# Kernel optimization log

Hardware: AMD Instinct MI355X
Metric: run time of the kernel (lower is better)

The kernel has to match this reference:

```python
import jax, jax.numpy as jnp
import numpy as np

N, E, G, D, L, T = 50000, 100000, 2000, 300, 5, 10
NUM_ATOM, NUM_CHIR, NUM_BOND, NUM_DIR = 120, 3, 6, 3


def setup_inputs() -> dict:
    key = jax.random.key(0)
    ks = jax.random.split(key, 24)
    s = 1.0 / np.sqrt(D)
    inp = {
        'x': jnp.stack([jax.random.randint(ks[0], (N,), 0, NUM_ATOM),
                        jax.random.randint(ks[1], (N,), 0, NUM_CHIR)], axis=1),
        'edge_index': jax.random.randint(ks[2], (2, E), 0, N),
        'edge_attr': jnp.stack([jax.random.randint(ks[3], (E,), 0, 4),
                                jax.random.randint(ks[4], (E,), 0, NUM_DIR)], axis=1),
        'batch': jnp.sort(jax.random.randint(ks[5], (N,), 0, G)),
        'x1': jnp.stack([jax.random.randint(ks[6], (N,), 0, NUM_ATOM),
                         jax.random.randint(ks[7], (N,), 0, NUM_CHIR)], axis=1),
        'edge_index1': jax.random.randint(ks[8], (2, E), 0, N),
        'edge_attr1': jnp.stack([jax.random.randint(ks[9], (E,), 0, 4),
                                 jax.random.randint(ks[10], (E,), 0, NUM_DIR)], axis=1),
        'batch1': jnp.sort(jax.random.randint(ks[11], (N,), 0, G)),
        'xemb1': jax.random.normal(ks[12], (NUM_ATOM, D)) * s,
        'xemb2': jax.random.normal(ks[13], (NUM_CHIR, D)) * s,
        'eemb1': jax.random.normal(ks[14], (L, NUM_BOND, D)) * s,
        'eemb2': jax.random.normal(ks[15], (L, NUM_DIR, D)) * s,
        'W1': jax.random.normal(ks[16], (L, D, 2 * D)) * s,
        'b1': jnp.zeros((L, 2 * D)),
        'W2': jax.random.normal(ks[17], (L, 2 * D, D)) * (1.0 / np.sqrt(2 * D)),
        'b2': jnp.zeros((L, D)),
        'gamma': jnp.ones((L, D)),
        'beta': jnp.zeros((L, D)),
        'predW': jax.random.normal(ks[18], (D, T)) * s,
        'predb': jnp.zeros((T,)),
    }
    return inp


def _gnn(xi, ei, ea, xemb1, xemb2, eemb1, eemb2, W1, b1, W2, b2, gamma, beta):
    n = xi.shape[0]
    h = xemb1[xi[:, 0]] + xemb2[xi[:, 1]]  # [N, D]
    loop = jnp.arange(n)
    src = jnp.concatenate([ei[0], loop])
    dst = jnp.concatenate([ei[1], loop])
    # self-loop edge attr = [4, 0]
    sl = jnp.concatenate([jnp.full((n, 1), 4, ea.dtype), jnp.zeros((n, 1), ea.dtype)], axis=1)
    eaf = jnp.concatenate([ea, sl], axis=0)
    for l in range(L):
        eemb = eemb1[l][eaf[:, 0]] + eemb2[l][eaf[:, 1]]     # [E+N, D]
        msg = h[src] + eemb                                   # gather
        agg = jax.ops.segment_sum(msg, dst, num_segments=n)   # scatter-add
        h2 = jax.nn.relu(agg @ W1[l] + b1[l]) @ W2[l] + b2[l] # GIN MLP
        mu = h2.mean(axis=0)
        var = ((h2 - mu) ** 2).mean(axis=0)                   # batchnorm (train stats)
        h2 = gamma[l] * (h2 - mu) * jax.lax.rsqrt(var + 1e-5) + beta[l]
        if l < L - 1:
            h2 = jax.nn.relu(h2)
        h = h2
    return h  # JK='last'


def _mean_pool(node_rep, batch):
    s = jax.ops.segment_sum(node_rep, batch, num_segments=G)
    cnt = jax.ops.segment_sum(jnp.ones((node_rep.shape[0],), node_rep.dtype), batch, num_segments=G)
    return s / jnp.maximum(cnt, 1.0)[:, None]


def reference(x, edge_index, edge_attr, batch, x1, edge_index1, edge_attr1, batch1,
              xemb1, xemb2, eemb1, eemb2, W1, b1, W2, b2, gamma, beta, predW, predb):
    node_rep = _gnn(x, edge_index, edge_attr, xemb1, xemb2, eemb1, eemb2, W1, b1, W2, b2, gamma, beta)
    node_rep1 = _gnn(x1, edge_index1, edge_attr1, xemb1, xemb2, eemb1, eemb2, W1, b1, W2, b2, gamma, beta)
    graph_rep = _mean_pool(node_rep, batch)
    graph_rep1 = _mean_pool(node_rep1, batch1)
    pred = graph_rep @ predW + predb
    pred1 = graph_rep1 @ predW + predb
    return (pred, graph_rep, node_rep, pred1, graph_rep1, node_rep1)
```

## Files before the change

kernel.cpp:

```cpp
#include <hip/hip_runtime.h>
#include <hip/hip_bf16.h>

typedef unsigned short ushort_t;
typedef short v8s __attribute__((ext_vector_type(8)));
typedef unsigned short v8u __attribute__((ext_vector_type(8)));
typedef unsigned short v4u __attribute__((ext_vector_type(4)));
typedef float v4f __attribute__((ext_vector_type(4)));

#define N_NODES 50000
#define N_EDGES 100000
#define N_GRAPH 2000
#define DIM     300
#define DIM2    600
#define NLAYER  5
#define NTASK   10
#define D4      75
#define D4P     80

#define LDA  304
#define LDY  608
#define LDAH 320
#define NPAD 50048

#define KB1 40
#define NT1 5
#define KB2 76
#define NT2 3
#define MT_TILES 391

#define AS1 __attribute__((address_space(1)))
#define AS3 __attribute__((address_space(3)))
static __device__ __forceinline__ void gload_lds16(const void* g, void* l) {
    __builtin_amdgcn_global_load_lds((AS1 void*)(g), (AS3 void*)(l), 16, 0, 0);
}

static __device__ __forceinline__ ushort_t f2bf(float f) {
    unsigned int u;
    __builtin_memcpy(&u, &f, 4);
    unsigned int lsb = (u >> 16) & 1u;
    u += 0x7fffu + lsb;
    return (ushort_t)(u >> 16);
}
static __device__ __forceinline__ void split2(float f, ushort_t& h, ushort_t& l) {
    unsigned int u;
    __builtin_memcpy(&u, &f, 4);
    h = (ushort_t)(u >> 16);
    unsigned int um = u & 0xFFFF0000u;
    float hf;
    __builtin_memcpy(&hf, &um, 4);
    float lf = f - hf;
    unsigned int ul;
    __builtin_memcpy(&ul, &lf, 4);
    l = (ushort_t)(ul >> 16);
}

static __device__ __forceinline__ int swz_wgid(int orig, int nwg) {
    int xcd = orig & 7;
    int seq = orig >> 3;
    int q = nwg >> 3, r = nwg & 7;
    int base = (xcd < r) ? xcd * (q + 1) : r * (q + 1) + (xcd - r) * q;
    return base + seq;
}

__global__ void k_embed_init(const int* __restrict__ x,
                             const float* __restrict__ xe1,
                             const float* __restrict__ xe2,
                             float* __restrict__ h) {
    int tid = blockIdx.x * blockDim.x + threadIdx.x;
    if (tid >= N_NODES * D4) return;
    int node = tid / D4;
    int d0 = (tid % D4) * 4;
    int i0 = x[node * 2 + 0];
    int i1 = x[node * 2 + 1];
    float4 a = *(const float4*)(xe1 + (size_t)i0 * DIM + d0);
    float4 b = *(const float4*)(xe2 + (size_t)i1 * DIM + d0);
    float4 o;
    o.x = a.x + b.x; o.y = a.y + b.y; o.z = a.z + b.z; o.w = a.w + b.w;
    *(float4*)(h + (size_t)node * LDA + d0) = o;
}

__global__ void k_deg(const int* __restrict__ ei, int* __restrict__ deg) {
    int e = blockIdx.x * blockDim.x + threadIdx.x;
    if (e >= N_EDGES) return;
    atomicAdd(&deg[ei[N_EDGES + e]], 1);
}

__global__ void k_scan1(const int* __restrict__ deg, int* __restrict__ excl,
                        int* __restrict__ blksum) {
    __shared__ int s[256];
    int i = blockIdx.x * 256 + threadIdx.x;
    int v = (i < N_NODES) ? deg[i] : 0;
    s[threadIdx.x] = v;
    __syncthreads();
#pragma unroll
    for (int o = 1; o < 256; o <<= 1) {
        int t = (threadIdx.x >= o) ? s[threadIdx.x - o] : 0;
        __syncthreads();
        s[threadIdx.x] += t;
        __syncthreads();
    }
    if (i < N_NODES) excl[i] = s[threadIdx.x] - v;
    if (threadIdx.x == 255) blksum[blockIdx.x] = s[255];
}

__global__ void k_scan2(int* __restrict__ blksum, int* __restrict__ blkoff, int nblk) {
    __shared__ int s[256];
    int v = (threadIdx.x < nblk) ? blksum[threadIdx.x] : 0;
    s[threadIdx.x] = v;
    __syncthreads();
#pragma unroll
    for (int o = 1; o < 256; o <<= 1) {
        int t = (threadIdx.x >= o) ? s[threadIdx.x - o] : 0;
        __syncthreads();
        s[threadIdx.x] += t;
        __syncthreads();
    }
    if (threadIdx.x < nblk) blkoff[threadIdx.x] = s[threadIdx.x] - v;
}

__global__ void k_scan3(const int* __restrict__ excl, const int* __restrict__ blkoff,
                        int* __restrict__ rowptr, int* __restrict__ fillptr) {
    int i = blockIdx.x * blockDim.x + threadIdx.x;
    if (i > N_NODES) return;
    int v = (i < N_NODES) ? (excl[i] + blkoff[i >> 8]) : N_EDGES;
    rowptr[i] = v;
    if (i < N_NODES) fillptr[i] = v;
}

__global__ void k_fill(const int* __restrict__ ei, const int* __restrict__ ea,
                       int* __restrict__ fillptr,
                       int* __restrict__ csrc, int* __restrict__ cea) {
    int e = blockIdx.x * blockDim.x + threadIdx.x;
    if (e >= N_EDGES) return;
    int dst = ei[N_EDGES + e];
    int pos = atomicAdd(&fillptr[dst], 1);
    csrc[pos] = ei[e];
    cea[pos] = (ea[2 * e + 0] << 16) | ea[2 * e + 1];
}

template <bool BN>
__global__ void k_gather_agg(const int* __restrict__ rowptr,
                             const int* __restrict__ csrc,
                             const int* __restrict__ cea,
                             const float* __restrict__ hin,
                             const float* __restrict__ ee1,
                             const float* __restrict__ ee2,
                             const float* __restrict__ ee1sl,
                             const float* __restrict__ ee2sl,
                             const float* __restrict__ bnmean,
                             const float* __restrict__ bnrstd,
                             const float* __restrict__ bngam,
                             const float* __restrict__ bnbet,
                             ushort_t* __restrict__ aghi,
                             ushort_t* __restrict__ aglo) {
    int tid = blockIdx.x * blockDim.x + threadIdx.x;
    if (tid >= N_NODES * D4P) return;
    int node = tid / D4P;
    int c = tid % D4P;
    if (c >= D4) {
        v4u z = (v4u){0, 0, 0, 0};
        *(v4u*)(aghi + (size_t)node * LDAH + c * 4) = z;
        *(v4u*)(aglo + (size_t)node * LDAH + c * 4) = z;
        return;
    }
    int d0 = c * 4;
    float4 m4, r4, g4, b4;
    if (BN) {
        m4 = *(const float4*)(bnmean + d0);
        r4 = *(const float4*)(bnrstd + d0);
        g4 = *(const float4*)(bngam + d0);
        b4 = *(const float4*)(bnbet + d0);
    }
    auto bn4 = [&](float4 v) -> float4 {
        if (BN) {
            v.x = fmaxf((v.x - m4.x) * r4.x * g4.x + b4.x, 0.f);
            v.y = fmaxf((v.y - m4.y) * r4.y * g4.y + b4.y, 0.f);
            v.z = fmaxf((v.z - m4.z) * r4.z * g4.z + b4.z, 0.f);
            v.w = fmaxf((v.w - m4.w) * r4.w * g4.w + b4.w, 0.f);
        }
        return v;
    };
    float4 a = bn4(*(const float4*)(hin + (size_t)node * LDA + d0));
    float4 e1 = *(const float4*)(ee1sl + d0);
    float4 e2 = *(const float4*)(ee2sl + d0);
    a.x += e1.x + e2.x; a.y += e1.y + e2.y; a.z += e1.z + e2.z; a.w += e1.w + e2.w;
    int p0 = rowptr[node], p1 = rowptr[node + 1];
    for (int p = p0; p < p1; ++p) {
        int src = csrc[p];
        int pk = cea[p];
        int a0 = pk >> 16, a1 = pk & 0xFFFF;
        float4 hv = bn4(*(const float4*)(hin + (size_t)src * LDA + d0));
        float4 f1 = *(const float4*)(ee1 + (size_t)a0 * DIM + d0);
        float4 f2 = *(const float4*)(ee2 + (size_t)a1 * DIM + d0);
        a.x += hv.x + f1.x + f2.x;
        a.y += hv.y + f1.y + f2.y;
        a.z += hv.z + f1.z + f2.z;
        a.w += hv.w + f1.w + f2.w;
    }
    float av[4] = {a.x, a.y, a.z, a.w};
    v4u hh, ll;
#pragma unroll
    for (int i = 0; i < 4; ++i) {
        ushort_t uh, ul;
        split2(av[i], uh, ul);
        hh[i] = uh;
        ll[i] = ul;
    }
    *(v4u*)(aghi + (size_t)node * LDAH + d0) = hh;
    *(v4u*)(aglo + (size_t)node * LDAH + d0) = ll;
}

__global__ void k_pack_w(const float* __restrict__ W,
                         ushort_t* __restrict__ hi,
                         ushort_t* __restrict__ lo,
                         int K, int N, int KBv, int NTv, int total) {
    int idx = blockIdx.x * blockDim.x + threadIdx.x;
    if (idx >= total) return;
    int j = idx & 7;
    int n = (idx >> 3) & 127;
    int tmp = idx >> 10;
    int kb = tmp % KBv; tmp /= KBv;
    int nt = tmp % NTv;
    int l = tmp / NTv;
    int k = kb * 8 + j;
    int ng = nt * 128 + n;
    float v = 0.f;
    if (k < K && ng < N) v = W[((size_t)l * K + k) * N + ng];
    ushort_t h, lw;
    split2(v, h, lw);
    hi[idx] = h;
    lo[idx] = lw;
}

template <bool RELU, bool SPLITA, bool BNSTAT, typename OT>
__global__ __launch_bounds__(256) void k_gemm_mfma(
        const ushort_t* __restrict__ Ahi,
        const ushort_t* __restrict__ Alo,
        const ushort_t* __restrict__ Bhi,
        const ushort_t* __restrict__ Blo,
        const float* __restrict__ bias,
        OT* __restrict__ C,
        double* __restrict__ bnsum,
        double* __restrict__ bnsq,
        int M, int N, int Ksteps, int KBv, int NTv, int nwg,
        int lda, int ldc, int ncap) {
    alignas(16) __shared__ ushort_t sAhi[8192];
    alignas(16) __shared__ ushort_t sAlo[SPLITA ? 8192 : 16];
    alignas(16) __shared__ ushort_t sBhi[8192];
    alignas(16) __shared__ ushort_t sBlo[8192];

    const int wgid = swz_wgid(blockIdx.x, nwg);
    const int nt = wgid % NTv;
    const int mt = wgid / NTv;
    const int t = threadIdx.x;

    const int w = t >> 6;
    const int lane = t & 63;
    const int wm = w >> 1;
    const int wn = w & 1;
    const int quad = lane >> 4;
    const int lr = lane & 15;

    v4f acc[4][4];
#pragma unroll
    for (int i = 0; i < 4; ++i)
#pragma unroll
        for (int j = 0; j < 4; ++j) acc[i][j] = (v4f){0.f, 0.f, 0.f, 0.f};

    auto stage = [&](int buf, int ks) {
        const int kk = ks * 32;
        const int bo = buf * 4096;
        const size_t base = ((size_t)nt * KBv + ks * 4) * 1024;
#pragma unroll
        for (int p = 0; p < 2; ++p) {
            int o = p * 2048 + t * 8;
            gload_lds16(Bhi + base + o, &sBhi[bo + o]);
            gload_lds16(Blo + base + o, &sBlo[bo + o]);
        }
#pragma unroll
        for (int p = 0; p < 2; ++p) {
            int cidx = p * 256 + t;
            int kb = cidx >> 7;
            int m = cidx & 127;
            size_t go = (size_t)(mt * 128 + m) * lda + kk + kb * 8;
            gload_lds16(Ahi + go, &sAhi[bo + cidx * 8]);
            if (SPLITA) gload_lds16(Alo + go, &sAlo[bo + cidx * 8]);
        }
    };

    stage(0, 0);
    __syncthreads();
    int cur = 0;
    for (int ks = 0; ks < Ksteps; ++ks) {
        if (ks + 1 < Ksteps) stage(cur ^ 1, ks + 1);
        const int bo = cur * 4096;
        v8s a_hi[4], a_lo[4];
#pragma unroll
        for (int s = 0; s < 4; ++s) {
            a_hi[s] = *(const v8s*)&sAhi[bo + quad * 1024 + (wm * 64 + s * 16 + lr) * 8];
            if (SPLITA)
                a_lo[s] = *(const v8s*)&sAlo[bo + quad * 1024 + (wm * 64 + s * 16 + lr) * 8];
        }
#pragma unroll
        for (int sj = 0; sj < 4; ++sj) {
            v8s bh = *(const v8s*)&sBhi[bo + quad * 1024 + (wn * 64 + sj * 16 + lr) * 8];
            v8s bl = *(const v8s*)&sBlo[bo + quad * 1024 + (wn * 64 + sj * 16 + lr) * 8];
#pragma unroll
            for (int si = 0; si < 4; ++si) {
                acc[si][sj] = __builtin_amdgcn_mfma_f32_16x16x32_bf16(
                    a_hi[si], bh, acc[si][sj], 0, 0, 0);
                acc[si][sj] = __builtin_amdgcn_mfma_f32_16x16x32_bf16(
                    a_hi[si], bl, acc[si][sj], 0, 0, 0);
                if (SPLITA)
                    acc[si][sj] = __builtin_amdgcn_mfma_f32_16x16x32_bf16(
                        a_lo[si], bh, acc[si][sj], 0, 0, 0);
            }
        }
        __syncthreads();
        cur ^= 1;
    }

    float bsum[4], bsq[4];
    if (BNSTAT) {
#pragma unroll
        for (int sj = 0; sj < 4; ++sj) { bsum[sj] = 0.f; bsq[sj] = 0.f; }
    }
#pragma unroll
    for (int sj = 0; sj < 4; ++sj) {
        int col = nt * 128 + wn * 64 + sj * 16 + lr;
        if (col >= ncap) continue;
        float bv = (col < N) ? bias[col] : 0.f;
#pragma unroll
        for (int si = 0; si < 4; ++si) {
#pragma unroll
            for (int r = 0; r < 4; ++r) {
                size_t row = (size_t)mt * 128 + wm * 64 + si * 16 + quad * 4 + r;
                float v = acc[si][sj][r] + bv;
                if (RELU) v = fmaxf(v, 0.f);
                if (BNSTAT && row < (size_t)M) { bsum[sj] += v; bsq[sj] += v * v; }
                if (sizeof(OT) == 2)
                    ((ushort_t*)C)[row * ldc + col] = f2bf(v);
                else
                    ((float*)C)[row * ldc + col] = v;
            }
        }
    }
    if (BNSTAT) {
        float* sred = (float*)sBhi;
#pragma unroll
        for (int sj = 0; sj < 4; ++sj) {
            bsum[sj] += __shfl_xor(bsum[sj], 16);
            bsum[sj] += __shfl_xor(bsum[sj], 32);
            bsq[sj]  += __shfl_xor(bsq[sj], 16);
            bsq[sj]  += __shfl_xor(bsq[sj], 32);
        }
        if (quad == 0) {
#pragma unroll
            for (int sj = 0; sj < 4; ++sj) {
                int idx = wm * 128 + wn * 64 + sj * 16 + lr;
                sred[idx] = bsum[sj];
                sred[256 + idx] = bsq[sj];
            }
        }
        __syncthreads();
        if (t < 128) {
            float s = sred[t] + sred[128 + t];
            float q = sred[256 + t] + sred[256 + 128 + t];
            int col = nt * 128 + t;
            if (col < N) {
                atomicAdd(&bnsum[col], (double)s);
                atomicAdd(&bnsq[col], (double)q);
            }
        }
    }
}

__global__ void k_bn_finalize(const double* __restrict__ sum,
                              const double* __restrict__ sumsq,
                              float* __restrict__ mean,
                              float* __restrict__ rstd) {
    int d = threadIdx.x;
    if (d >= DIM) return;
    double mu = sum[d] / (double)N_NODES;
    double var = sumsq[d] / (double)N_NODES - mu * mu;
    if (var < 0.0) var = 0.0;
    mean[d] = (float)mu;
    rstd[d] = (float)(1.0 / sqrt(var + 1e-5));
}

__global__ __launch_bounds__(256) void k_bn_pool(const float* __restrict__ h2,
                                                 const int* __restrict__ batch,
                                                 const float* __restrict__ mean,
                                                 const float* __restrict__ rstd,
                                                 const float* __restrict__ gam,
                                                 const float* __restrict__ bet,
                                                 float* __restrict__ nodeout,
                                                 float* __restrict__ pool,
                                                 float* __restrict__ gout) {
    __shared__ float4 s[3][D4];
    const int g = blockIdx.x;
    int lo = 0, hi = N_NODES;
    while (lo < hi) {
        int m = (lo + hi) >> 1;
        if (batch[m] < g) lo = m + 1; else hi = m;
    }
    const int p0 = lo;
    hi = N_NODES;
    while (lo < hi) {
        int m = (lo + hi) >> 1;
        if (batch[m] < g + 1) lo = m + 1; else hi = m;
    }
    const int p1 = lo;

    const int t = threadIdx.x;
    if (t < 3 * D4) {
        const int c = t % D4;
        const int rc = t / D4;
        const int d0 = c * 4;
        float4 m4 = *(const float4*)(mean + d0);
        float4 r4 = *(const float4*)(rstd + d0);
        float4 g4 = *(const float4*)(gam + d0);
        float4 b4 = *(const float4*)(bet + d0);
        float4 acc = {0.f, 0.f, 0.f, 0.f};
        for (int r = p0 + rc; r < p1; r += 3) {
            float4 v = *(const float4*)(h2 + (size_t)r * LDA + d0);
            v.x = (v.x - m4.x) * r4.x * g4.x + b4.x;
            v.y = (v.y - m4.y) * r4.y * g4.y + b4.y;
            v.z = (v.z - m4.z) * r4.z * g4.z + b4.z;
            v.w = (v.w - m4.w) * r4.w * g4.w + b4.w;
            *(float4*)(nodeout + (size_t)r * DIM + d0) = v;
            acc.x += v.x; acc.y += v.y; acc.z += v.z; acc.w += v.w;
        }
        s[rc][c] = acc;
    }
    __syncthreads();
    if (t < D4) {
        float4 a = s[0][t], b = s[1][t], c = s[2][t];
        const float inv = 1.0f / fmaxf((float)(p1 - p0), 1.0f);
        float4 r;
        r.x = (a.x + b.x + c.x) * inv;
        r.y = (a.y + b.y + c.y) * inv;
        r.z = (a.z + b.z + c.z) * inv;
        r.w = (a.w + b.w + c.w) * inv;
        *(float4*)(pool + (size_t)g * DIM + t * 4) = r;
        *(float4*)(gout + (size_t)g * DIM + t * 4) = r;
    }
}

__global__ void k_pred(const float* __restrict__ pool,
                       const float* __restrict__ predW,
                       const float* __restrict__ predb,
                       float* __restrict__ out) {
    int tid = blockIdx.x * blockDim.x + threadIdx.x;
    if (tid >= N_GRAPH * NTASK) return;
    int g = tid / NTASK;
    int tt = tid % NTASK;
    float s = predb[tt];
    const float* pr = pool + (size_t)g * DIM;
    for (int k = 0; k < DIM; ++k) s += pr[k] * predW[k * NTASK + tt];
    out[(size_t)g * NTASK + tt] = s;
}

static inline int cdiv(long long a, long long b) { return (int)((a + b - 1) / b); }

extern "C" void kernel_launch(void* const* d_in, const int* in_sizes, int n_in,
                              void* d_out, int out_size, void* d_ws, size_t ws_size,
                              hipStream_t stream) {
    const int* x    = (const int*)d_in[0];
    const int* ei   = (const int*)d_in[1];
    const int* ea   = (const int*)d_in[2];
    const int* bat  = (const int*)d_in[3];
    const int* x1   = (const int*)d_in[4];
    const int* ei1  = (const int*)d_in[5];
    const int* ea1  = (const int*)d_in[6];
    const int* bat1 = (const int*)d_in[7];
    const float* xemb1 = (const float*)d_in[8];
    const float* xemb2 = (const float*)d_in[9];
    const float* eemb1 = (const float*)d_in[10];
    const float* eemb2 = (const float*)d_in[11];
    const float* W1    = (const float*)d_in[12];
    const float* b1    = (const float*)d_in[13];
    const float* W2    = (const float*)d_in[14];
    const float* b2    = (const float*)d_in[15];
    const float* gamma = (const float*)d_in[16];
    const float* beta  = (const float*)d_in[17];
    const float* predW = (const float*)d_in[18];
    const float* predb = (const float*)d_in[19];
    float* out = (float*)d_out;

    char* ws = (char*)d_ws;
    size_t off = 0;
    auto take = [&](size_t bytes) -> char* {
        char* p = ws + off;
        off += (bytes + 255) & ~(size_t)255;
        return p;
    };
    const size_t BUFSZ = (size_t)NPAD * LDAH * 2 * 2;
    char* bufA = take(BUFSZ);
    char* bufB = take(BUFSZ);
    float* pool   = (float*)take((size_t)N_GRAPH * DIM * 4);
    double* bnsum = (double*)take(DIM * 8 * 2);
    double* bnsq  = bnsum + DIM;
    float* bnmean = (float*)take(DIM * 4 * 2);
    float* bnrstd = bnmean + DIM;
    const size_t W1P = (size_t)NLAYER * NT1 * KB1 * 1024;
    const size_t W2P = (size_t)NLAYER * NT2 * KB2 * 1024;
    ushort_t* w1hi = (ushort_t*)take(W1P * 2);
    ushort_t* w1lo = (ushort_t*)take(W1P * 2);
    ushort_t* w2hi = (ushort_t*)take(W2P * 2);
    ushort_t* w2lo = (ushort_t*)take(W2P * 2);
    int* deg     = (int*)take(N_NODES * 4);
    int* excl    = (int*)take(N_NODES * 4);
    int* blksum  = (int*)take(256 * 4);
    int* blkoff  = (int*)take(256 * 4);
    int* fillptr = (int*)take(N_NODES * 4);
    int* rowptr0 = (int*)take((N_NODES + 1) * 4);
    int* csrc0   = (int*)take(N_EDGES * 4);
    int* cea0    = (int*)take(N_EDGES * 4);
    int* rowptr1 = (int*)take((N_NODES + 1) * 4);
    int* csrc1   = (int*)take(N_EDGES * 4);
    int* cea1    = (int*)take(N_EDGES * 4);
    (void)ws_size; (void)in_sizes; (void)n_in; (void)out_size;

    const int TB = 256;
    const int gN75 = cdiv((long long)N_NODES * D4, TB);
    const int gN80 = cdiv((long long)N_NODES * D4P, TB);
    const int gE   = cdiv(N_EDGES, TB);
    const int gScan = cdiv(N_NODES, TB);
    const int gScan3 = cdiv(N_NODES + 1, TB);
    const int NWG1 = NT1 * MT_TILES;
    const int NWG2 = NT2 * MT_TILES;

    k_pack_w<<<cdiv((long long)W1P, TB), TB, 0, stream>>>(W1, w1hi, w1lo, DIM, DIM2, KB1, NT1, (int)W1P);
    k_pack_w<<<cdiv((long long)W2P, TB), TB, 0, stream>>>(W2, w2hi, w2lo, DIM2, DIM, KB2, NT2, (int)W2P);

    auto build_csr = [&](const int* eip, const int* eap, int* rowptr, int* csrc, int* cea) {
        hipMemsetAsync(deg, 0, N_NODES * 4, stream);
        k_deg<<<gE, TB, 0, stream>>>(eip, deg);
        k_scan1<<<gScan, TB, 0, stream>>>(deg, excl, blksum);
        k_scan2<<<1, 256, 0, stream>>>(blksum, blkoff, gScan);
        k_scan3<<<gScan3, TB, 0, stream>>>(excl, blkoff, rowptr, fillptr);
        k_fill<<<gE, TB, 0, stream>>>(eip, eap, fillptr, csrc, cea);
    };
    build_csr(ei, ea, rowptr0, csrc0, cea0);
    build_csr(ei1, ea1, rowptr1, csrc1, cea1);

    auto run_gnn = [&](const int* xp, const int* batp,
                       const int* rowptr, const int* csrc, const int* cea,
                       float* out_pred, float* out_graph, float* out_node) {
        k_embed_init<<<gN75, TB, 0, stream>>>(xp, xemb1, xemb2, (float*)bufA);
        for (int l = 0; l < NLAYER; ++l) {
            char* pb = (l & 1) ? bufA : bufB;
            char* yb = (l & 1) ? bufB : bufA;
            ushort_t* aghi = (ushort_t*)pb;
            ushort_t* aglo = aghi + (size_t)NPAD * LDAH;
            const float* gin = (const float*)yb;
            ushort_t* yv = (ushort_t*)yb;
            float* h2v = (float*)pb;
            const float* ee1l = eemb1 + (size_t)l * 6 * DIM;
            const float* ee2l = eemb2 + (size_t)l * 3 * DIM;
            if (l == 0)
                k_gather_agg<false><<<gN80, TB, 0, stream>>>(
                    rowptr, csrc, cea, gin, ee1l, ee2l, ee1l + 4 * DIM, ee2l,
                    nullptr, nullptr, nullptr, nullptr, aghi, aglo);
            else
                k_gather_agg<true><<<gN80, TB, 0, stream>>>(
                    rowptr, csrc, cea, gin, ee1l, ee2l, ee1l + 4 * DIM, ee2l,
                    bnmean, bnrstd, gamma + (size_t)(l - 1) * DIM, beta + (size_t)(l - 1) * DIM,
                    aghi, aglo);
            k_gemm_mfma<true, true, false, ushort_t>
                <<<NWG1, TB, 0, stream>>>(
                    aghi, aglo,
                    w1hi + (size_t)l * NT1 * KB1 * 1024, w1lo + (size_t)l * NT1 * KB1 * 1024,
                    b1 + (size_t)l * DIM2, yv, nullptr, nullptr,
                    N_NODES, DIM2, 10, KB1, NT1, NWG1, LDAH, LDY, LDY);
            hipMemsetAsync(bnsum, 0, DIM * 8 * 2, stream);
            k_gemm_mfma<false, false, true, float>
                <<<NWG2, TB, 0, stream>>>(
                    yv, yv,
                    w2hi + (size_t)l * NT2 * KB2 * 1024, w2lo + (size_t)l * NT2 * KB2 * 1024,
                    b2 + (size_t)l * DIM, h2v, bnsum, bnsq,
                    N_NODES, DIM, 19, KB2, NT2, NWG2, LDY, LDA, LDA);
            k_bn_finalize<<<1, 512, 0, stream>>>(bnsum, bnsq, bnmean, bnrstd);
        }
        k_bn_pool<<<N_GRAPH, TB, 0, stream>>>(
            (const float*)bufB, batp, bnmean, bnrstd,
            gamma + (size_t)(NLAYER - 1) * DIM, beta + (size_t)(NLAYER - 1) * DIM,
            out_node, pool, out_graph);
        k_pred<<<cdiv((long long)N_GRAPH * NTASK, TB), TB, 0, stream>>>(pool, predW, predb, out_pred);
    };

    const size_t GT = (size_t)N_GRAPH * NTASK;
    const size_t GD = (size_t)N_GRAPH * DIM;
    const size_t ND = (size_t)N_NODES * DIM;
    run_gnn(x, bat, rowptr0, csrc0, cea0, out, out + GT, out + GT + GD);
    run_gnn(x1, bat1, rowptr1, csrc1, cea1,
            out + GT + GD + ND, out + 2 * GT + GD + ND, out + 2 * GT + 2 * GD + ND);
}
```

Measured before the change: 2.167 ms.

## Store GEMM A operands in pre-tiled blocked layout for contiguous LDS loads

The gather kernel and the first GEMM's bf16 output now write activations in a tile-blocked layout of 128 rows by 32 k. Each GEMM stage can then load a contiguous 8 KB A chunk, matching how B is already packed, instead of strided row loads. The per-layer bnsum memset is dropped: finalize zeroes the accumulators after reading them, with one memset up front. The cost is scattered 8-byte and 2-byte stores in the producer kernels, which may coalesce less well.

New measurement: 2.098 ms. 1.03x faster.

```diff
diff --git a/kernel.cpp b/kernel.cpp
--- a/kernel.cpp
+++ b/kernel.cpp
@@ -18,9 +18,9 @@
 #define D4P     80
 
 #define LDA  304
-#define LDY  608
-#define LDAH 320
 #define NPAD 50048
+#define KST1 10
+#define KST2 19
 
 #define KB1 40
 #define NT1 5
@@ -157,13 +157,16 @@
     if (tid >= N_NODES * D4P) return;
     int node = tid / D4P;
     int c = tid % D4P;
+    int d0 = c * 4;
+    const int mt = node >> 7, m = node & 127;
+    const int ks = d0 >> 5, kb = (d0 >> 3) & 3, jq = d0 & 7;
+    const size_t off = (((size_t)mt * KST1 + ks) * 4 + kb) * 1024 + m * 8 + jq;
     if (c >= D4) {
         v4u z = (v4u){0, 0, 0, 0};
-        *(v4u*)(aghi + (size_t)node * LDAH + c * 4) = z;
-        *(v4u*)(aglo + (size_t)node * LDAH + c * 4) = z;
+        *(v4u*)(aghi + off) = z;
+        *(v4u*)(aglo + off) = z;
         return;
     }
-    int d0 = c * 4;
     float4 m4, r4, g4, b4;
     if (BN) {
         m4 = *(const float4*)(bnmean + d0);
@@ -206,8 +209,8 @@
         hh[i] = uh;
         ll[i] = ul;
     }
-    *(v4u*)(aghi + (size_t)node * LDAH + d0) = hh;
-    *(v4u*)(aglo + (size_t)node * LDAH + d0) = ll;
+    *(v4u*)(aghi + off) = hh;
+    *(v4u*)(aglo + off) = ll;
 }
 
 __global__ void k_pack_w(const float* __restrict__ W,
@@ -243,7 +246,7 @@
         double* __restrict__ bnsum,
         double* __restrict__ bnsq,
         int M, int N, int Ksteps, int KBv, int NTv, int nwg,
-        int lda, int ldc, int ncap) {
+        int ldc, int ncap, int ksout) {
     alignas(16) __shared__ ushort_t sAhi[8192];
     alignas(16) __shared__ ushort_t sAlo[SPLITA ? 8192 : 16];
     alignas(16) __shared__ ushort_t sBhi[8192];
@@ -268,23 +271,16 @@
         for (int j = 0; j < 4; ++j) acc[i][j] = (v4f){0.f, 0.f, 0.f, 0.f};
 
     auto stage = [&](int buf, int ks) {
-        const int kk = ks * 32;
         const int bo = buf * 4096;
-        const size_t base = ((size_t)nt * KBv + ks * 4) * 1024;
+        const size_t bbase = ((size_t)nt * KBv + ks * 4) * 1024;
+        const size_t abase = ((size_t)mt * Ksteps + ks) * 4096;
 #pragma unroll
         for (int p = 0; p < 2; ++p) {
             int o = p * 2048 + t * 8;
-            gload_lds16(Bhi + base + o, &sBhi[bo + o]);
-            gload_lds16(Blo + base + o, &sBlo[bo + o]);
-        }
-#pragma unroll
-        for (int p = 0; p < 2; ++p) {
-            int cidx = p * 256 + t;
-            int kb = cidx >> 7;
-            int m = cidx & 127;
-            size_t go = (size_t)(mt * 128 + m) * lda + kk + kb * 8;
-            gload_lds16(Ahi + go, &sAhi[bo + cidx * 8]);
-            if (SPLITA) gload_lds16(Alo + go, &sAlo[bo + cidx * 8]);
+            gload_lds16(Bhi + bbase + o, &sBhi[bo + o]);
+            gload_lds16(Blo + bbase + o, &sBlo[bo + o]);
+            gload_lds16(Ahi + abase + o, &sAhi[bo + o]);
+            if (SPLITA) gload_lds16(Alo + abase + o, &sAlo[bo + o]);
         }
     };
 
@@ -330,16 +326,20 @@
         int col = nt * 128 + wn * 64 + sj * 16 + lr;
         if (col >= ncap) continue;
         float bv = (col < N) ? bias[col] : 0.f;
+        size_t yb = 0;
+        if (sizeof(OT) == 2)
+            yb = (((size_t)mt * ksout + (col >> 5)) * 4 + ((col >> 3) & 3)) * 1024 + (col & 7);
 #pragma unroll
         for (int si = 0; si < 4; ++si) {
 #pragma unroll
             for (int r = 0; r < 4; ++r) {
-                size_t row = (size_t)mt * 128 + wm * 64 + si * 16 + quad * 4 + r;
+                int m = wm * 64 + si * 16 + quad * 4 + r;
+                size_t row = (size_t)mt * 128 + m;
                 float v = acc[si][sj][r] + bv;
                 if (RELU) v = fmaxf(v, 0.f);
                 if (BNSTAT && row < (size_t)M) { bsum[sj] += v; bsq[sj] += v * v; }
                 if (sizeof(OT) == 2)
-                    ((ushort_t*)C)[row * ldc + col] = f2bf(v);
+                    ((ushort_t*)C)[yb + m * 8] = f2bf(v);
                 else
                     ((float*)C)[row * ldc + col] = v;
             }
@@ -375,8 +375,8 @@
     }
 }
 
-__global__ void k_bn_finalize(const double* __restrict__ sum,
-                              const double* __restrict__ sumsq,
+__global__ void k_bn_finalize(double* __restrict__ sum,
+                              double* __restrict__ sumsq,
                               float* __restrict__ mean,
                               float* __restrict__ rstd) {
     int d = threadIdx.x;
@@ -386,6 +386,8 @@
     if (var < 0.0) var = 0.0;
     mean[d] = (float)mu;
     rstd[d] = (float)(1.0 / sqrt(var + 1e-5));
+    sum[d] = 0.0;
+    sumsq[d] = 0.0;
 }
 
 __global__ __launch_bounds__(256) void k_bn_pool(const float* __restrict__ h2,
@@ -495,7 +497,8 @@
         off += (bytes + 255) & ~(size_t)255;
         return p;
     };
-    const size_t BUFSZ = (size_t)NPAD * LDAH * 2 * 2;
+    const size_t PLANE = (size_t)MT_TILES * KST1 * 4096;
+    const size_t BUFSZ = PLANE * 2 * 2;
     char* bufA = take(BUFSZ);
     char* bufB = take(BUFSZ);
     float* pool   = (float*)take((size_t)N_GRAPH * DIM * 4);
@@ -545,6 +548,8 @@
     build_csr(ei, ea, rowptr0, csrc0, cea0);
     build_csr(ei1, ea1, rowptr1, csrc1, cea1);
 
+    hipMemsetAsync(bnsum, 0, DIM * 8 * 2, stream);
+
     auto run_gnn = [&](const int* xp, const int* batp,
                        const int* rowptr, const int* csrc, const int* cea,
                        float* out_pred, float* out_graph, float* out_node) {
@@ -553,7 +558,7 @@
             char* pb = (l & 1) ? bufA : bufB;
             char* yb = (l & 1) ? bufB : bufA;
             ushort_t* aghi = (ushort_t*)pb;
-            ushort_t* aglo = aghi + (size_t)NPAD * LDAH;
+            ushort_t* aglo = aghi + PLANE;
             const float* gin = (const float*)yb;
             ushort_t* yv = (ushort_t*)yb;
             float* h2v = (float*)pb;
@@ -573,14 +578,13 @@
                     aghi, aglo,
                     w1hi + (size_t)l * NT1 * KB1 * 1024, w1lo + (size_t)l * NT1 * KB1 * 1024,
                     b1 + (size_t)l * DIM2, yv, nullptr, nullptr,
-                    N_NODES, DIM2, 10, KB1, NT1, NWG1, LDAH, LDY, LDY);
-            hipMemsetAsync(bnsum, 0, DIM * 8 * 2, stream);
+                    N_NODES, DIM2, KST1, KB1, NT1, NWG1, 0, 608, KST2);
             k_gemm_mfma<false, false, true, float>
                 <<<NWG2, TB, 0, stream>>>(
                     yv, yv,
                     w2hi + (size_t)l * NT2 * KB2 * 1024, w2lo + (size_t)l * NT2 * KB2 * 1024,
                     b2 + (size_t)l * DIM, h2v, bnsum, bnsq,
-                    N_NODES, DIM, 19, KB2, NT2, NWG2, LDY, LDA, LDA);
+                    N_NODES, DIM, KST2, KB2, NT2, NWG2, LDA, 304, 0);
             k_bn_finalize<<<1, 512, 0, stream>>>(bnsum, bnsq, bnmean, bnrstd);
         }
         k_bn_pool<<<N_GRAPH, TB, 0, stream>>>(
```
